# Performance work log

Hardware: AMD Instinct MI355X
Metric: run time of the kernel (lower is better)

Reference implementation:

```python
import jax, jax.numpy as jnp
import numpy as np

ATT_DIM = 2048
NUM_HEADS = 16
NUM_KV_GROUPS = 4
HEAD_DIM = 128
CONTEXT_LENGTH = 2048
ROPE_BASE = 10000.0
GROUP_SIZE = NUM_HEADS // NUM_KV_GROUPS
BATCH = 2


def _precompute_rope_sin(context_length, head_dim, rope_base):
    # thetas over rope_dim = head_dim // 2, exponent uses rope_dim (as in source)
    rope_dim = head_dim // 2
    j = jnp.arange(rope_dim, dtype=jnp.float32)
    thetas = 1.0 / rope_base ** (2.0 * j / rope_dim)
    positions = jnp.arange(context_length, dtype=jnp.float32)
    angles = positions[:, None] * thetas[None, :]          # [CD, HD//2]
    angles = jnp.concatenate([angles, angles], axis=-1)    # [CD, HD]
    return jnp.sin(angles)                                  # cos is unused (see bug note)


def _apply_rope(qk, sin):
    # FAITHFUL to source bug: in compute_rope, `cos` is overwritten with the
    # broadcast `sin`, so the returned value is qk*sin + qk_2*sin.
    hd = qk.shape[-1]
    qkr = qk[..., : hd // 2]
    qki = qk[..., hd // 2 :]
    qk2 = jnp.concatenate([-qki, qkr], axis=-1)
    sin_b = sin[None, None, : qk.shape[2], :]
    return qk * sin_b + qk2 * sin  # second term broadcasts full-length sin (requires cd==context_length)


def setup_inputs() -> dict:
    key = jax.random.key(0)
    ks = jax.random.split(key, 6)
    s = 0.02
    x = jax.random.normal(ks[0], (BATCH, CONTEXT_LENGTH, ATT_DIM), dtype=jnp.float32)
    Wq = jax.random.normal(ks[1], (ATT_DIM, HEAD_DIM * NUM_HEADS), dtype=jnp.float32) * s
    Wk = jax.random.normal(ks[2], (ATT_DIM, HEAD_DIM * NUM_KV_GROUPS), dtype=jnp.float32) * s
    Wv = jax.random.normal(ks[3], (ATT_DIM, HEAD_DIM * NUM_KV_GROUPS), dtype=jnp.float32) * s
    Wo = jax.random.normal(ks[4], (HEAD_DIM * NUM_HEADS, HEAD_DIM * NUM_HEADS), dtype=jnp.float32) * s
    bo = jax.random.normal(ks[5], (HEAD_DIM * NUM_HEADS,), dtype=jnp.float32) * s
    return {"x": x, "Wq": Wq, "Wk": Wk, "Wv": Wv, "Wo": Wo, "bo": bo}


def reference(x, Wq, Wk, Wv, Wo, bo):
    bd, cd, ed = x.shape
    sin = _precompute_rope_sin(CONTEXT_LENGTH, HEAD_DIM, ROPE_BASE)

    q = (x @ Wq).reshape(bd, cd, NUM_HEADS, HEAD_DIM).transpose(0, 2, 1, 3)      # [B,NH,CD,HD]
    k = (x @ Wk).reshape(bd, cd, NUM_KV_GROUPS, HEAD_DIM).transpose(0, 2, 1, 3)  # [B,Nkv,CD,HD]
    v = (x @ Wv).reshape(bd, cd, NUM_KV_GROUPS, HEAD_DIM).transpose(0, 2, 1, 3)

    q = _apply_rope(q, sin)
    k = _apply_rope(k, sin)

    k = jnp.repeat(k, GROUP_SIZE, axis=1)  # [B,NH,CD,HD]
    v = jnp.repeat(v, GROUP_SIZE, axis=1)

    a = jnp.einsum("bhqd,bhkd->bhqk", q, k)  # [B,NH,CD,CD]
    causal = jnp.triu(jnp.ones((cd, cd), dtype=bool), k=1)
    a = jnp.where(causal[None, None], -jnp.inf, a)
    a = jax.nn.softmax(a / jnp.sqrt(jnp.float32(HEAD_DIM)), axis=-1)

    y = jnp.einsum("bhqk,bhkd->bhqd", a, v)                # [B,NH,CD,HD]
    y = y.transpose(0, 2, 1, 3).reshape(bd, cd, HEAD_DIM * NUM_HEADS)
    return y @ Wo + bo
```

## Files before the change

kernel.cpp:

```cpp
#include <hip/hip_runtime.h>
#include <hip/hip_bf16.h>
#include <cstdint>
#include <cstddef>

#define BATCH 2
#define CTX 2048
#define EMB 2048
#define NH 16
#define NG 4
#define HD 128
#define NQK (EMB + 2*NG*HD)
#define MROWS (BATCH*CTX)

typedef __bf16 bf16x8 __attribute__((ext_vector_type(8)));
typedef float  f32x4  __attribute__((ext_vector_type(4)));
typedef float  f32x16 __attribute__((ext_vector_type(16)));

__device__ __forceinline__ ushort f2bf(float f) {
    uint32_t u = __float_as_uint(f);
    u += 0x7FFFu + ((u >> 16) & 1u);
    return (ushort)(u >> 16);
}

__device__ __forceinline__ float bf2f(ushort u) {
    return __uint_as_float((uint32_t)u << 16);
}

__device__ __forceinline__ uint32_t packbf(float a, float b) {
    ushort lo = __builtin_bit_cast(ushort, (__bf16)a);
    ushort hi = __builtin_bit_cast(ushort, (__bf16)b);
    return (uint32_t)lo | ((uint32_t)hi << 16);
}

__device__ __forceinline__ bf16x8 mkfrag(uint32_t a, uint32_t b, uint32_t c, uint32_t d) {
    union { uint32_t u[4]; bf16x8 v; } z;
    z.u[0] = a; z.u[1] = b; z.u[2] = c; z.u[3] = d;
    return z.v;
}

__device__ __forceinline__ void gload_lds16(const void* g, void* l) {
    __builtin_amdgcn_global_load_lds((const __attribute__((address_space(1))) void*)g,
                                     (__attribute__((address_space(3))) void*)l, 16, 0, 0);
}

__global__ __launch_bounds__(256) void k_sintab(float* __restrict__ sintab) {
    int t = blockIdx.x * 256 + threadIdx.x;
    int j = t & 63, p = t >> 6;
    float theta = 1.0f / powf(10000.0f, (float)(2 * j) / 64.0f);
    sintab[t] = sinf((float)p * theta);
}

__global__ __launch_bounds__(256) void k_cvt(const float4* __restrict__ src, ushort4* __restrict__ dst) {
    int i = blockIdx.x * 256 + threadIdx.x;
    float4 v = src[i];
    ushort4 o;
    o.x = f2bf(v.x); o.y = f2bf(v.y); o.z = f2bf(v.z); o.w = f2bf(v.w);
    dst[i] = o;
}

__global__ __launch_bounds__(256) void k_transpose_cvt(const float* __restrict__ src, int src_ld,
                                                       ushort* __restrict__ dst, int dst_ld) {
    __shared__ float tile[32][33];
    int tx = threadIdx.x, ty = threadIdx.y;
    int c0 = blockIdx.x * 32, r0 = blockIdx.y * 32;
    #pragma unroll
    for (int i = 0; i < 4; ++i)
        tile[ty + i*8][tx] = src[(size_t)(r0 + ty + i*8) * src_ld + c0 + tx];
    __syncthreads();
    #pragma unroll
    for (int i = 0; i < 4; ++i)
        dst[(size_t)(c0 + ty + i*8) * dst_ld + r0 + tx] = f2bf(tile[tx][ty + i*8]);
}

__global__ __launch_bounds__(256) void k_rope_q(const ushort* __restrict__ qkv,
                                                const float* __restrict__ sintab, ushort* __restrict__ out,
                                                float qs) {
    int t = blockIdx.x * 256 + threadIdx.x;
    int j = t & 63;
    int rest = t >> 6;
    int pos = rest & (CTX - 1);
    int rest2 = rest >> 11;
    int hh = rest2 % NH;
    int b = rest2 / NH;
    const ushort* base = qkv + (size_t)(b * CTX + pos) * NQK + hh * HD;
    float a  = bf2f(base[j]);
    float bb = bf2f(base[j + 64]);
    float sv = sintab[pos * 64 + j] * qs;
    ushort* ob = out + ((size_t)((b * NH + hh) * CTX + pos)) * HD;
    ob[j]      = f2bf((a - bb) * sv);
    ob[j + 64] = f2bf((bb + a) * sv);
}

__global__ __launch_bounds__(256) void k_rope_kf(const ushort* __restrict__ qkv,
                                                 const float* __restrict__ sintab, ushort* __restrict__ Kf) {
    int t = blockIdx.x * 256 + threadIdx.x;
    int j = t & 63;
    int rest = t >> 6;
    int pos = rest & (CTX - 1);
    int rest2 = rest >> 11;
    int g = rest2 % NG;
    int b = rest2 / NG;
    int bg = b * NG + g;
    const ushort* base = qkv + (size_t)(b * CTX + pos) * NQK + EMB + g * HD;
    float a  = bf2f(base[j]);
    float bb = bf2f(base[j + 64]);
    float sv = sintab[pos * 64 + j];
    size_t idx0 = (size_t)(bg * 64 + (pos >> 5)) * 4096
                + (size_t)(j >> 4) * 512 + ((j >> 3) & 1) * 256 + (pos & 31) * 8 + (j & 7);
    Kf[idx0]        = f2bf((a - bb) * sv);
    Kf[idx0 + 2048] = f2bf((bb + a) * sv);
}

__global__ __launch_bounds__(256) void k_vfrag(const ushort* __restrict__ qkvb, ushort* __restrict__ Vf) {
    int lane = threadIdx.x;
    int dt   = threadIdx.y;
    int step = blockIdx.x;
    int bg   = blockIdx.y;
    int b = bg >> 2, g = bg & 3;
    int ln = lane & 31, hi = lane >> 5;
    int col = EMB + NG*HD + g*HD + dt*32 + ln;
    #pragma unroll
    for (int ks = 0; ks < 2; ++ks) {
        int pos0 = step*32 + ks*16 + hi*8;
        ushort v[8];
        #pragma unroll
        for (int e = 0; e < 8; ++e)
            v[e] = qkvb[(size_t)(b*CTX + pos0 + e) * NQK + col];
        union { uint32_t u[4]; bf16x8 bv; } z;
        z.u[0] = (uint32_t)v[0] | ((uint32_t)v[1] << 16);
        z.u[1] = (uint32_t)v[2] | ((uint32_t)v[3] << 16);
        z.u[2] = (uint32_t)v[4] | ((uint32_t)v[5] << 16);
        z.u[3] = (uint32_t)v[6] | ((uint32_t)v[7] << 16);
        *(bf16x8*)(Vf + ((size_t)(bg*64 + step)*8 + dt*2 + ks) * 512 + lane*8) = z.bv;
    }
}

template<bool BF16OUT>
__global__ __launch_bounds__(256) void k_gemm_bt(const ushort* __restrict__ A, const ushort* __restrict__ Bt,
                                                 void* __restrict__ Cv, int M, int N, int K,
                                                 const float* __restrict__ bias) {
    __shared__ __align__(16) ushort As[2][128 * 32];
    __shared__ __align__(16) ushort Bs[2][128 * 32];
    int tid = threadIdx.x;
    int lane = tid & 63;
    int wave = tid >> 6;
    int wr = wave >> 1, wc = wave & 1;
    int m0 = blockIdx.y * 128, n0 = blockIdx.x * 128;
    int lr = lane & 15, lg = lane >> 4;

    f32x4 acc[4][4] = {};

    int arow = lane >> 2;
    int kpart = (lane & 3) * 8;

    int nsteps = K >> 5;

    #pragma unroll
    for (int s = 0; s < 2; ++s) {
        int c = wave * 2 + s;
        gload_lds16(A  + (size_t)(m0 + c*16 + arow) * K + kpart, &As[0][c * 512]);
        gload_lds16(Bt + (size_t)(n0 + c*16 + arow) * K + kpart, &Bs[0][c * 512]);
    }
    __syncthreads();

    for (int t = 0; t < nsteps; ++t) {
        int cur = t & 1;
        if (t + 1 < nsteps) {
            int k1 = (t + 1) << 5;
            #pragma unroll
            for (int s = 0; s < 2; ++s) {
                int c = wave * 2 + s;
                gload_lds16(A  + (size_t)(m0 + c*16 + arow) * K + k1 + kpart, &As[cur ^ 1][c * 512]);
                gload_lds16(Bt + (size_t)(n0 + c*16 + arow) * K + k1 + kpart, &Bs[cur ^ 1][c * 512]);
            }
        }
        bf16x8 af[4], bfr[4];
        #pragma unroll
        for (int mt = 0; mt < 4; ++mt)
            af[mt] = *(const bf16x8*)&As[cur][(wr*64 + mt*16 + lr) * 32 + lg * 8];
        #pragma unroll
        for (int nt = 0; nt < 4; ++nt)
            bfr[nt] = *(const bf16x8*)&Bs[cur][(wc*64 + nt*16 + lr) * 32 + lg * 8];
        #pragma unroll
        for (int mt = 0; mt < 4; ++mt)
            #pragma unroll
            for (int nt = 0; nt < 4; ++nt)
                acc[mt][nt] = __builtin_amdgcn_mfma_f32_16x16x32_bf16(af[mt], bfr[nt], acc[mt][nt], 0, 0, 0);
        __syncthreads();
    }

    #pragma unroll
    for (int mt = 0; mt < 4; ++mt) {
        #pragma unroll
        for (int nt = 0; nt < 4; ++nt) {
            int col = n0 + wc*64 + nt*16 + lr;
            float bv = bias ? bias[col] : 0.0f;
            #pragma unroll
            for (int r = 0; r < 4; ++r) {
                int row = m0 + wr*64 + mt*16 + lg*4 + r;
                float v = acc[mt][nt][r] + bv;
                if constexpr (BF16OUT)
                    ((ushort*)Cv)[(size_t)row * N + col] = f2bf(v);
                else
                    ((float*)Cv)[(size_t)row * N + col] = v;
            }
        }
    }
}

__global__ __launch_bounds__(128) void k_attn7(const ushort* __restrict__ Qb, const ushort* __restrict__ Kf,
                                               const ushort* __restrict__ Vf, ushort* __restrict__ y) {
    __shared__ __align__(16) char smem[16640];
    char*  Qs  = smem;
    float* sOd = (float*)smem;
    float* sm  = (float*)(smem + 16384);
    float* sl  = (float*)(smem + 16512);

    int lane = threadIdx.x & 63;
    int w    = threadIdx.x >> 6;
    int B  = blockIdx.x;
    int bg = B & 7;
    int within = B >> 3;
    int t  = 63 - (within >> 2);
    int hh = within & 3;
    int b = bg >> 2, g = bg & 3, h = g * 4 + hh;
    int ln = lane & 31, hi = lane >> 5;
    int q0 = t * 32;

    {
        int r  = threadIdx.x >> 2;
        int c0 = threadIdx.x & 3;
        const ushort* qg = Qb + ((size_t)((b*NH + h) * CTX) + q0 + r) * HD;
        #pragma unroll
        for (int it = 0; it < 4; ++it) {
            int c = c0 + it * 4;
            bf16x8 v = *(const bf16x8*)(qg + c * 8);
            *(bf16x8*)(Qs + r * 256 + ((c ^ (r & 7)) * 16)) = v;
        }
    }
    __syncthreads();

    const ushort* kfb = Kf + (size_t)bg * 64 * 4096 + lane * 8;
    const ushort* vfb = Vf + (size_t)bg * 64 * 4096 + lane * 8;

    f32x16 od[4] = {};
    float m = -1e30f, lsum = 0.0f;

    int nsteps = t + 1;
    for (int si = w; si < nsteps; si += 2) {
        const ushort* kp = kfb + (size_t)si * 4096;
        const ushort* vp = vfb + (size_t)si * 4096;
        f32x16 st = {};
        #pragma unroll
        for (int s = 0; s < 8; ++s) {
            bf16x8 kf = *(const bf16x8*)(kp + s * 512);
            bf16x8 qf = *(const bf16x8*)(Qs + ln * 256 + (((2*s + hi) ^ (ln & 7)) * 16));
            st = __builtin_amdgcn_mfma_f32_32x32x16_bf16(kf, qf, st, 0, 0, 0);
        }

        if (si == t) {
            #pragma unroll
            for (int r = 0; r < 16; ++r) {
                int kl = (r & 3) + 8*(r >> 2) + 4*hi;
                if (kl > ln) st[r] = -1e30f;
            }
        }
        float m8[8];
        #pragma unroll
        for (int r = 0; r < 8; ++r) m8[r] = fmaxf(st[r], st[r+8]);
        #pragma unroll
        for (int r = 0; r < 4; ++r) m8[r] = fmaxf(m8[r], m8[r+4]);
        float pmax = fmaxf(fmaxf(m8[0], m8[1]), fmaxf(m8[2], m8[3]));
        pmax = fmaxf(pmax, __shfl_xor(pmax, 32, 64));

        if (!__all(pmax <= m + 8.0f)) {
            float mnew = fmaxf(m, pmax);
            float alpha = exp2f(m - mnew);
            lsum *= alpha;
            m = mnew;
            #pragma unroll
            for (int r = 0; r < 16; ++r) {
                float ar = __shfl(alpha, (r & 3) + 8*(r >> 2) + 4*hi, 64);
                #pragma unroll
                for (int dt = 0; dt < 4; ++dt) od[dt][r] *= ar;
            }
        }
        float ls = 0.0f;
        #pragma unroll
        for (int r = 0; r < 16; ++r) { st[r] = exp2f(st[r] - m); ls += st[r]; }
        lsum += ls + __shfl_xor(ls, 32, 64);

        #pragma unroll
        for (int ks = 0; ks < 2; ++ks) {
            uint32_t w0 = packbf(st[8*ks+0], st[8*ks+1]);
            uint32_t w1 = packbf(st[8*ks+2], st[8*ks+3]);
            uint32_t w2 = packbf(st[8*ks+4], st[8*ks+5]);
            uint32_t w3 = packbf(st[8*ks+6], st[8*ks+7]);
            uint32_t x0 = (uint32_t)__shfl_xor((int)w0, 32, 64);
            uint32_t x1 = (uint32_t)__shfl_xor((int)w1, 32, 64);
            uint32_t x2 = (uint32_t)__shfl_xor((int)w2, 32, 64);
            uint32_t x3 = (uint32_t)__shfl_xor((int)w3, 32, 64);
            bf16x8 pa = hi ? mkfrag(x2, x3, w2, w3) : mkfrag(w0, w1, x0, x1);
            #pragma unroll
            for (int dt = 0; dt < 4; ++dt) {
                bf16x8 vf = *(const bf16x8*)(vp + (dt*2 + ks) * 512);
                od[dt] = __builtin_amdgcn_mfma_f32_32x32x16_bf16(pa, vf, od[dt], 0, 0, 0);
            }
        }
    }

    __syncthreads();
    if (w == 1) {
        #pragma unroll
        for (int r = 0; r < 16; ++r) {
            int ri = (r & 3) + 8*(r >> 2) + 4*hi;
            #pragma unroll
            for (int dt = 0; dt < 4; ++dt) sOd[ri*128 + dt*32 + ln] = od[dt][r];
        }
        if (hi == 0) { sm[ln] = m; sl[ln] = lsum; }
    }
    __syncthreads();
    if (w == 0) {
        float m1 = sm[ln], l1 = sl[ln];
        float mnew = fmaxf(m, m1);
        float a0 = exp2f(m - mnew);
        float a1 = exp2f(m1 - mnew);
        float inv = 1.0f / (lsum * a0 + l1 * a1);
        #pragma unroll
        for (int r = 0; r < 16; ++r) {
            int ri = (r & 3) + 8*(r >> 2) + 4*hi;
            float a0r = __shfl(a0, ri, 64);
            float a1r = __shfl(a1, ri, 64);
            float ivr = __shfl(inv, ri, 64);
            int row = q0 + ri;
            #pragma unroll
            for (int dt = 0; dt < 4; ++dt) {
                float v = (od[dt][r] * a0r + sOd[ri*128 + dt*32 + ln] * a1r) * ivr;
                y[((size_t)(b*CTX + row)) * (NH*HD) + h*HD + dt*32 + ln] = f2bf(v);
            }
        }
    }
}

#define SIN_OFF   ((size_t)0)
#define XB_OFF    ((size_t)524288)
#define WT_OFF    ((size_t)17301504)
#define WOT_OFF   ((size_t)29884416)
#define QKV_OFF   ((size_t)38273024)
#define QB_OFF    ((size_t)88604672)
#define KB_OFF    ((size_t)105381888)
#define VT_OFF    ((size_t)109576192)
#define YB_OFF    ((size_t)113770496)

extern "C" void kernel_launch(void* const* d_in, const int* in_sizes, int n_in,
                              void* d_out, int out_size, void* d_ws, size_t ws_size,
                              hipStream_t stream) {
    const float* x  = (const float*)d_in[0];
    const float* Wq = (const float*)d_in[1];
    const float* Wk = (const float*)d_in[2];
    const float* Wv = (const float*)d_in[3];
    const float* Wo = (const float*)d_in[4];
    const float* bo = (const float*)d_in[5];
    float* out = (float*)d_out;
    char* ws = (char*)d_ws;

    float*  sintab = (float*)(ws + SIN_OFF);
    ushort* xb     = (ushort*)(ws + XB_OFF);
    ushort* Wt     = (ushort*)(ws + WT_OFF);
    ushort* Wot    = (ushort*)(ws + WOT_OFF);
    ushort* QKVb   = (ushort*)(ws + QKV_OFF);
    ushort* Qb     = (ushort*)(ws + QB_OFF);
    ushort* Kf     = (ushort*)(ws + KB_OFF);
    ushort* Vf     = (ushort*)(ws + VT_OFF);
    ushort* yb     = (ushort*)(ws + YB_OFF);

    k_sintab<<<512, 256, 0, stream>>>(sintab);
    k_cvt<<<(MROWS * EMB / 4) / 256, 256, 0, stream>>>((const float4*)x, (ushort4*)xb);
    dim3 tb(32, 8);
    k_transpose_cvt<<<dim3(EMB/32, EMB/32), tb, 0, stream>>>(Wq, EMB, Wt, EMB);
    k_transpose_cvt<<<dim3((NG*HD)/32, EMB/32), tb, 0, stream>>>(Wk, NG*HD, Wt + (size_t)EMB * EMB, EMB);
    k_transpose_cvt<<<dim3((NG*HD)/32, EMB/32), tb, 0, stream>>>(Wv, NG*HD, Wt + (size_t)(EMB + NG*HD) * EMB, EMB);
    k_transpose_cvt<<<dim3(EMB/32, EMB/32), tb, 0, stream>>>(Wo, EMB, Wot, EMB);
    k_gemm_bt<true><<<dim3(NQK/128, MROWS/128), 256, 0, stream>>>(xb, Wt, QKVb, MROWS, NQK, EMB, nullptr);
    const float qscale = 0.08838834764831845f * 1.4426950408889634f;
    k_rope_q <<<(BATCH*NH*CTX*64)/256, 256, 0, stream>>>(QKVb, sintab, Qb, qscale);
    k_rope_kf<<<(BATCH*NG*CTX*64)/256, 256, 0, stream>>>(QKVb, sintab, Kf);
    k_vfrag<<<dim3(64, BATCH*NG), dim3(64, 4), 0, stream>>>(QKVb, Vf);
    k_attn7<<<2048, 128, 0, stream>>>(Qb, Kf, Vf, yb);
    k_gemm_bt<false><<<dim3(EMB/128, MROWS/128), 256, 0, stream>>>(yb, Wot, out, MROWS, EMB, EMB, bo);
}
```

Before: 235.6 us.

## Split attention KV loop across four waves with tree reduction of partials

```diff
diff --git a/kernel.cpp b/kernel.cpp
--- a/kernel.cpp
+++ b/kernel.cpp
@@ -208,16 +208,20 @@
     }
 }
 
-__global__ __launch_bounds__(128) void k_attn7(const ushort* __restrict__ Qb, const ushort* __restrict__ Kf,
+__global__ __launch_bounds__(256) void k_attn8(const ushort* __restrict__ Qb, const ushort* __restrict__ Kf,
                                                const ushort* __restrict__ Vf, ushort* __restrict__ y) {
-    __shared__ __align__(16) char smem[16640];
-    char*  Qs  = smem;
-    float* sOd = (float*)smem;
-    float* sm  = (float*)(smem + 16384);
-    float* sl  = (float*)(smem + 16512);
-
-    int lane = threadIdx.x & 63;
-    int w    = threadIdx.x >> 6;
+    __shared__ __align__(16) char smem[33280];
+    char*  Qs   = smem;
+    float* buf0 = (float*)smem;
+    float* buf1 = (float*)(smem + 16384);
+    float* sm0  = (float*)(smem + 32768);
+    float* sl0  = (float*)(smem + 32896);
+    float* sm1  = (float*)(smem + 33024);
+    float* sl1  = (float*)(smem + 33152);
+
+    int tid  = threadIdx.x;
+    int lane = tid & 63;
+    int w    = tid >> 6;
     int B  = blockIdx.x;
     int bg = B & 7;
     int within = B >> 3;
@@ -228,12 +232,12 @@
     int q0 = t * 32;
 
     {
-        int r  = threadIdx.x >> 2;
-        int c0 = threadIdx.x & 3;
+        int r  = tid >> 3;
+        int c0 = tid & 7;
         const ushort* qg = Qb + ((size_t)((b*NH + h) * CTX) + q0 + r) * HD;
         #pragma unroll
-        for (int it = 0; it < 4; ++it) {
-            int c = c0 + it * 4;
+        for (int it = 0; it < 2; ++it) {
+            int c = c0 + it * 8;
             bf16x8 v = *(const bf16x8*)(qg + c * 8);
             *(bf16x8*)(Qs + r * 256 + ((c ^ (r & 7)) * 16)) = v;
         }
@@ -247,7 +251,7 @@
     float m = -1e30f, lsum = 0.0f;
 
     int nsteps = t + 1;
-    for (int si = w; si < nsteps; si += 2) {
+    for (int si = w; si < nsteps; si += 4) {
         const ushort* kp = kfb + (size_t)si * 4096;
         const ushort* vp = vfb + (size_t)si * 4096;
         f32x16 st = {};
@@ -310,18 +314,51 @@
     }
 
     __syncthreads();
-    if (w == 1) {
+    if (w & 1) {
+        float* bufp = (w == 1) ? buf0 : buf1;
         #pragma unroll
         for (int r = 0; r < 16; ++r) {
             int ri = (r & 3) + 8*(r >> 2) + 4*hi;
             #pragma unroll
-            for (int dt = 0; dt < 4; ++dt) sOd[ri*128 + dt*32 + ln] = od[dt][r];
-        }
-        if (hi == 0) { sm[ln] = m; sl[ln] = lsum; }
+            for (int dt = 0; dt < 4; ++dt) bufp[ri*128 + dt*32 + ln] = od[dt][r];
+        }
+        if (hi == 0) {
+            if (w == 1) { sm0[ln] = m; sl0[ln] = lsum; }
+            else        { sm1[ln] = m; sl1[ln] = lsum; }
+        }
+    }
+    __syncthreads();
+    if ((w & 1) == 0) {
+        float* bufp = (w == 0) ? buf0 : buf1;
+        float m1 = (w == 0) ? sm0[ln] : sm1[ln];
+        float l1 = (w == 0) ? sl0[ln] : sl1[ln];
+        float mnew = fmaxf(m, m1);
+        float a0 = exp2f(m - mnew);
+        float a1 = exp2f(m1 - mnew);
+        lsum = lsum * a0 + l1 * a1;
+        m = mnew;
+        #pragma unroll
+        for (int r = 0; r < 16; ++r) {
+            int ri = (r & 3) + 8*(r >> 2) + 4*hi;
+            float a0r = __shfl(a0, ri, 64);
+            float a1r = __shfl(a1, ri, 64);
+            #pragma unroll
+            for (int dt = 0; dt < 4; ++dt)
+                od[dt][r] = od[dt][r] * a0r + bufp[ri*128 + dt*32 + ln] * a1r;
+        }
+        if (w == 2) {
+            #pragma unroll
+            for (int r = 0; r < 16; ++r) {
+                int ri = (r & 3) + 8*(r >> 2) + 4*hi;
+                #pragma unroll
+                for (int dt = 0; dt < 4; ++dt) buf1[ri*128 + dt*32 + ln] = od[dt][r];
+            }
+            if (hi == 0) { sm1[ln] = m; sl1[ln] = lsum; }
+        }
     }
     __syncthreads();
     if (w == 0) {
-        float m1 = sm[ln], l1 = sl[ln];
+        float m1 = sm1[ln], l1 = sl1[ln];
         float mnew = fmaxf(m, m1);
         float a0 = exp2f(m - mnew);
         float a1 = exp2f(m1 - mnew);
@@ -335,7 +372,7 @@
             int row = q0 + ri;
             #pragma unroll
             for (int dt = 0; dt < 4; ++dt) {
-                float v = (od[dt][r] * a0r + sOd[ri*128 + dt*32 + ln] * a1r) * ivr;
+                float v = (od[dt][r] * a0r + buf1[ri*128 + dt*32 + ln] * a1r) * ivr;
                 y[((size_t)(b*CTX + row)) * (NH*HD) + h*HD + dt*32 + ln] = f2bf(v);
             }
         }
@@ -386,6 +423,6 @@
     k_rope_q <<<(BATCH*NH*CTX*64)/256, 256, 0, stream>>>(QKVb, sintab, Qb, qscale);
     k_rope_kf<<<(BATCH*NG*CTX*64)/256, 256, 0, stream>>>(QKVb, sintab, Kf);
     k_vfrag<<<dim3(64, BATCH*NG), dim3(64, 4), 0, stream>>>(QKVb, Vf);
-    k_attn7<<<2048, 128, 0, stream>>>(Qb, Kf, Vf, yb);
+    k_attn8<<<2048, 256, 0, stream>>>(Qb, Kf, Vf, yb);
     k_gemm_bt<false><<<dim3(EMB/128, MROWS/128), 256, 0, stream>>>(yb, Wot, out, MROWS, EMB, EMB, bo);
 }
```

New measurement: 242.4 us. 1.03x slower.

## Store Q in MFMA fragment layout, merge rope kernels, add setprio around MFMAs

Applied to the files above, without the earlier changes.

```diff
diff --git a/kernel.cpp b/kernel.cpp
--- a/kernel.cpp
+++ b/kernel.cpp
@@ -72,43 +72,36 @@
         dst[(size_t)(c0 + ty + i*8) * dst_ld + r0 + tx] = f2bf(tile[tx][ty + i*8]);
 }
 
-__global__ __launch_bounds__(256) void k_rope_q(const ushort* __restrict__ qkv,
-                                                const float* __restrict__ sintab, ushort* __restrict__ out,
+__global__ __launch_bounds__(256) void k_rope_f(const ushort* __restrict__ qkv,
+                                                const float* __restrict__ sintab,
+                                                ushort* __restrict__ Qf, ushort* __restrict__ Kf,
                                                 float qs) {
     int t = blockIdx.x * 256 + threadIdx.x;
     int j = t & 63;
     int rest = t >> 6;
     int pos = rest & (CTX - 1);
     int rest2 = rest >> 11;
-    int hh = rest2 % NH;
-    int b = rest2 / NH;
-    const ushort* base = qkv + (size_t)(b * CTX + pos) * NQK + hh * HD;
+    int u = rest2 % (NH + NG);
+    int b = rest2 / (NH + NG);
+    const ushort* base;
+    ushort* dst;
+    float scale;
+    if (u < NH) {
+        base = qkv + (size_t)(b * CTX + pos) * NQK + u * HD;
+        dst = Qf + (size_t)((b * NH + u) * 64 + (pos >> 5)) * 4096;
+        scale = qs;
+    } else {
+        int g = u - NH;
+        base = qkv + (size_t)(b * CTX + pos) * NQK + EMB + g * HD;
+        dst = Kf + (size_t)((b * NG + g) * 64 + (pos >> 5)) * 4096;
+        scale = 1.0f;
+    }
     float a  = bf2f(base[j]);
     float bb = bf2f(base[j + 64]);
-    float sv = sintab[pos * 64 + j] * qs;
-    ushort* ob = out + ((size_t)((b * NH + hh) * CTX + pos)) * HD;
-    ob[j]      = f2bf((a - bb) * sv);
-    ob[j + 64] = f2bf((bb + a) * sv);
-}
-
-__global__ __launch_bounds__(256) void k_rope_kf(const ushort* __restrict__ qkv,
-                                                 const float* __restrict__ sintab, ushort* __restrict__ Kf) {
-    int t = blockIdx.x * 256 + threadIdx.x;
-    int j = t & 63;
-    int rest = t >> 6;
-    int pos = rest & (CTX - 1);
-    int rest2 = rest >> 11;
-    int g = rest2 % NG;
-    int b = rest2 / NG;
-    int bg = b * NG + g;
-    const ushort* base = qkv + (size_t)(b * CTX + pos) * NQK + EMB + g * HD;
-    float a  = bf2f(base[j]);
-    float bb = bf2f(base[j + 64]);
-    float sv = sintab[pos * 64 + j];
-    size_t idx0 = (size_t)(bg * 64 + (pos >> 5)) * 4096
-                + (size_t)(j >> 4) * 512 + ((j >> 3) & 1) * 256 + (pos & 31) * 8 + (j & 7);
-    Kf[idx0]        = f2bf((a - bb) * sv);
-    Kf[idx0 + 2048] = f2bf((bb + a) * sv);
+    float sv = sintab[pos * 64 + j] * scale;
+    size_t idx0 = (size_t)(j >> 4) * 512 + ((j >> 3) & 1) * 256 + (pos & 31) * 8 + (j & 7);
+    dst[idx0]        = f2bf((a - bb) * sv);
+    dst[idx0 + 2048] = f2bf((bb + a) * sv);
 }
 
 __global__ __launch_bounds__(256) void k_vfrag(const ushort* __restrict__ qkvb, ushort* __restrict__ Vf) {
@@ -208,7 +201,7 @@
     }
 }
 
-__global__ __launch_bounds__(128) void k_attn7(const ushort* __restrict__ Qb, const ushort* __restrict__ Kf,
+__global__ __launch_bounds__(128) void k_attn9(const ushort* __restrict__ Qf, const ushort* __restrict__ Kf,
                                                const ushort* __restrict__ Vf, ushort* __restrict__ y) {
     __shared__ __align__(16) char smem[16640];
     char*  Qs  = smem;
@@ -228,37 +221,35 @@
     int q0 = t * 32;
 
     {
-        int r  = threadIdx.x >> 2;
-        int c0 = threadIdx.x & 3;
-        const ushort* qg = Qb + ((size_t)((b*NH + h) * CTX) + q0 + r) * HD;
-        #pragma unroll
-        for (int it = 0; it < 4; ++it) {
-            int c = c0 + it * 4;
-            bf16x8 v = *(const bf16x8*)(qg + c * 8);
-            *(bf16x8*)(Qs + r * 256 + ((c ^ (r & 7)) * 16)) = v;
-        }
+        const ushort* qf_g = Qf + ((size_t)((b*NH + h) * 64 + t)) * 4096;
+        int tid = threadIdx.x;
+        #pragma unroll
+        for (int it = 0; it < 4; ++it)
+            gload_lds16(qf_g + (it*128 + tid) * 8, Qs + it*2048 + w*1024);
     }
     __syncthreads();
 
     const ushort* kfb = Kf + (size_t)bg * 64 * 4096 + lane * 8;
     const ushort* vfb = Vf + (size_t)bg * 64 * 4096 + lane * 8;
+    const char*   qsl = Qs + lane * 16;
 
     f32x16 od[4] = {};
     float m = -1e30f, lsum = 0.0f;
 
-    int nsteps = t + 1;
-    for (int si = w; si < nsteps; si += 2) {
+    auto step = [&](int si, bool diag) {
         const ushort* kp = kfb + (size_t)si * 4096;
         const ushort* vp = vfb + (size_t)si * 4096;
         f32x16 st = {};
+        __builtin_amdgcn_s_setprio(1);
         #pragma unroll
         for (int s = 0; s < 8; ++s) {
             bf16x8 kf = *(const bf16x8*)(kp + s * 512);
-            bf16x8 qf = *(const bf16x8*)(Qs + ln * 256 + (((2*s + hi) ^ (ln & 7)) * 16));
+            bf16x8 qf = *(const bf16x8*)(qsl + s * 1024);
             st = __builtin_amdgcn_mfma_f32_32x32x16_bf16(kf, qf, st, 0, 0, 0);
         }
-
-        if (si == t) {
+        __builtin_amdgcn_s_setprio(0);
+
+        if (diag) {
             #pragma unroll
             for (int r = 0; r < 16; ++r) {
                 int kl = (r & 3) + 8*(r >> 2) + 4*hi;
@@ -268,9 +259,9 @@
         float m8[8];
         #pragma unroll
         for (int r = 0; r < 8; ++r) m8[r] = fmaxf(st[r], st[r+8]);
-        #pragma unroll
-        for (int r = 0; r < 4; ++r) m8[r] = fmaxf(m8[r], m8[r+4]);
-        float pmax = fmaxf(fmaxf(m8[0], m8[1]), fmaxf(m8[2], m8[3]));
+        float m4a = fmaxf(fmaxf(m8[0], m8[1]), m8[2]);
+        float m4b = fmaxf(fmaxf(m8[3], m8[4]), m8[5]);
+        float pmax = fmaxf(fmaxf(m4a, m4b), fmaxf(m8[6], m8[7]));
         pmax = fmaxf(pmax, __shfl_xor(pmax, 32, 64));
 
         if (!__all(pmax <= m + 8.0f)) {
@@ -285,9 +276,14 @@
                 for (int dt = 0; dt < 4; ++dt) od[dt][r] *= ar;
             }
         }
-        float ls = 0.0f;
-        #pragma unroll
-        for (int r = 0; r < 16; ++r) { st[r] = exp2f(st[r] - m); ls += st[r]; }
+        #pragma unroll
+        for (int r = 0; r < 16; ++r) st[r] = exp2f(st[r] - m);
+        float s8[8];
+        #pragma unroll
+        for (int r = 0; r < 8; ++r) s8[r] = st[r] + st[r+8];
+        #pragma unroll
+        for (int r = 0; r < 4; ++r) s8[r] = s8[r] + s8[r+4];
+        float ls = (s8[0] + s8[1]) + (s8[2] + s8[3]);
         lsum += ls + __shfl_xor(ls, 32, 64);
 
         #pragma unroll
@@ -301,13 +297,18 @@
             uint32_t x2 = (uint32_t)__shfl_xor((int)w2, 32, 64);
             uint32_t x3 = (uint32_t)__shfl_xor((int)w3, 32, 64);
             bf16x8 pa = hi ? mkfrag(x2, x3, w2, w3) : mkfrag(w0, w1, x0, x1);
+            __builtin_amdgcn_s_setprio(1);
             #pragma unroll
             for (int dt = 0; dt < 4; ++dt) {
                 bf16x8 vf = *(const bf16x8*)(vp + (dt*2 + ks) * 512);
                 od[dt] = __builtin_amdgcn_mfma_f32_32x32x16_bf16(pa, vf, od[dt], 0, 0, 0);
             }
-        }
-    }
+            __builtin_amdgcn_s_setprio(0);
+        }
+    };
+
+    for (int si = w; si < t; si += 2) step(si, false);
+    if ((t & 1) == w) step(t, true);
 
     __syncthreads();
     if (w == 1) {
@@ -369,7 +370,7 @@
     ushort* Wt     = (ushort*)(ws + WT_OFF);
     ushort* Wot    = (ushort*)(ws + WOT_OFF);
     ushort* QKVb   = (ushort*)(ws + QKV_OFF);
-    ushort* Qb     = (ushort*)(ws + QB_OFF);
+    ushort* Qf     = (ushort*)(ws + QB_OFF);
     ushort* Kf     = (ushort*)(ws + KB_OFF);
     ushort* Vf     = (ushort*)(ws + VT_OFF);
     ushort* yb     = (ushort*)(ws + YB_OFF);
@@ -383,9 +384,8 @@
     k_transpose_cvt<<<dim3(EMB/32, EMB/32), tb, 0, stream>>>(Wo, EMB, Wot, EMB);
     k_gemm_bt<true><<<dim3(NQK/128, MROWS/128), 256, 0, stream>>>(xb, Wt, QKVb, MROWS, NQK, EMB, nullptr);
     const float qscale = 0.08838834764831845f * 1.4426950408889634f;
-    k_rope_q <<<(BATCH*NH*CTX*64)/256, 256, 0, stream>>>(QKVb, sintab, Qb, qscale);
-    k_rope_kf<<<(BATCH*NG*CTX*64)/256, 256, 0, stream>>>(QKVb, sintab, Kf);
+    k_rope_f<<<(BATCH*(NH+NG)*CTX*64)/256, 256, 0, stream>>>(QKVb, sintab, Qf, Kf, qscale);
     k_vfrag<<<dim3(64, BATCH*NG), dim3(64, 4), 0, stream>>>(QKVb, Vf);
-    k_attn7<<<2048, 128, 0, stream>>>(Qb, Kf, Vf, yb);
+    k_attn9<<<2048, 128, 0, stream>>>(Qf, Kf, Vf, yb);
     k_gemm_bt<false><<<dim3(EMB/128, MROWS/128), 256, 0, stream>>>(yb, Wot, out, MROWS, EMB, EMB, bo);
 }
```

Measured after the change: 266.0 us. +12.9%, slower.
